# Kernel optimization log

Measured on AMD Instinct MI355X. Metric: run time of the kernel, lower is better.

## Reference

```python
import jax, jax.numpy as jnp
import numpy as np

N_NODES = 50000
N_EDGES = 800000
N_GRAPHS = 512
HID = 128
N_LAYERS = 4
EPS = 1e-4


def setup_inputs() -> dict:
    key = jax.random.key(0)
    ks = jax.random.split(key, 20)
    s = 0.05
    return {
        "z": jax.random.randint(ks[0], (N_NODES,), 0, 100),
        "pos": jax.random.normal(ks[1], (N_NODES, 3), jnp.float32),
        "batch": jnp.sort(jax.random.randint(ks[2], (N_NODES,), 0, N_GRAPHS)),
        "edge_index": jax.random.randint(ks[3], (2, N_EDGES), 0, N_NODES),
        "embed_tab": jax.random.normal(ks[4], (100, HID), jnp.float32) * s,
        "W_pos": jax.random.normal(ks[5], (3, HID), jnp.float32) * s,
        "b_pos": jax.random.normal(ks[6], (HID,), jnp.float32) * s,
        "W_comb": jax.random.normal(ks[7], (2 * HID, HID), jnp.float32) * s,
        "b_comb": jax.random.normal(ks[8], (HID,), jnp.float32) * s,
        "gin_W1": jax.random.normal(ks[9], (N_LAYERS, HID, HID), jnp.float32) * s,
        "gin_b1": jax.random.normal(ks[10], (N_LAYERS, HID), jnp.float32) * s,
        "gin_W2": jax.random.normal(ks[11], (N_LAYERS, HID, HID), jnp.float32) * s,
        "gin_b2": jax.random.normal(ks[12], (N_LAYERS, HID), jnp.float32) * s,
        # heads stacked in order: [alpha, beta, nu, gamma]
        "head_W1": jax.random.normal(ks[13], (4, HID, HID), jnp.float32) * s,
        "head_b1": jax.random.normal(ks[14], (4, HID), jnp.float32) * s,
        "head_W2": jax.random.normal(ks[15], (4, HID, 1), jnp.float32) * s,
        "head_b2": jax.random.normal(ks[16], (4, 1), jnp.float32) * s,
    }


def _forward(z, pos, batch, edge_index, embed_tab, W_pos, b_pos, W_comb, b_comb,
             gin_W1, gin_b1, gin_W2, gin_b2, head_W1, head_b1, head_W2, head_b2):
    # initial embedding: atom embed + linear pos embed -> combine MLP
    atom = embed_tab[z]                                    # [N, H]
    pemb = pos @ W_pos + b_pos                             # [N, H]
    x = jax.nn.relu(jnp.concatenate([atom, pemb], -1) @ W_comb + b_comb)
    src, dst = edge_index[0], edge_index[1]
    # GIN stack: h = MLP(x + sum_{j in N(i)} x_j); ReLU between convs, none after last
    for l in range(N_LAYERS):
        agg = jax.ops.segment_sum(x[src], dst, num_segments=N_NODES)  # [N, H]
        h = x + agg                                        # eps = 0
        h = jax.nn.relu(h @ gin_W1[l] + gin_b1[l]) @ gin_W2[l] + gin_b2[l]
        x = jax.nn.relu(h) if l < N_LAYERS - 1 else h
    # sum pooling per graph
    aggr = jax.ops.segment_sum(x, batch, num_segments=N_GRAPHS)  # [G, F]
    # 4 heads (alpha, beta, nu, gamma), each Linear-ReLU-Linear -> [4, G, 1]
    hh = jax.nn.relu(jnp.einsum('gh,khf->kgf', aggr, head_W1) + head_b1[:, None, :])
    out = jnp.einsum('kgf,kfo->kgo', hh, head_W2) + head_b2[:, None, :]
    alpha = jnp.maximum(jax.nn.softplus(out[0]) + 1.0, 1.0 + EPS)
    beta = jax.nn.softplus(out[1])
    nu = jax.nn.softplus(out[2])
    gamma = out[3]
    aleatoric = beta / (alpha - 1.0)
    epistemic = beta / ((alpha - 1.0) * nu)
    return (gamma, aleatoric, epistemic, nu, alpha, beta)


def reference(z, pos, batch, edge_index, embed_tab, W_pos, b_pos, W_comb, b_comb,
              gin_W1, gin_b1, gin_W2, gin_b2, head_W1, head_b1, head_W2, head_b2):
    return _forward(z, pos, batch, edge_index, embed_tab, W_pos, b_pos, W_comb,
                    b_comb, gin_W1, gin_b1, gin_W2, gin_b2, head_W1, head_b1,
                    head_W2, head_b2)
```

## Files before the change

### kernel.cpp

```cpp
#include <hip/hip_runtime.h>
#include <stdint.h>

#define NN 50000
#define NE 800000
#define NG 512
#define H  128
#define NBK 196
#define EPB 3125

typedef __attribute__((ext_vector_type(8))) short short8;
typedef __attribute__((ext_vector_type(16))) float f32x16;
typedef __attribute__((ext_vector_type(2))) float float2v;

union U4S8 { uint4 u; short8 s; };

__device__ __forceinline__ float softplusf(float x){
    return fmaxf(x, 0.f) + log1pf(expf(-fabsf(x)));
}

__device__ __forceinline__ unsigned rne_bf16_hi(float x){
    unsigned u = __float_as_uint(x);
    unsigned r = u + 0x7fffu + ((u >> 16) & 1u);
    return r & 0xffff0000u;
}

__device__ __forceinline__ void split_pack(float x0, float x1, unsigned &hi, unsigned &lo){
    unsigned h0 = rne_bf16_hi(x0), h1 = rne_bf16_hi(x1);
    hi = (h0 >> 16) | h1;
    float l0 = x0 - __uint_as_float(h0);
    float l1 = x1 - __uint_as_float(h1);
    unsigned g0 = rne_bf16_hi(l0), g1 = rne_bf16_hi(l1);
    lo = (g0 >> 16) | g1;
}

__global__ void k_sentinel(float* out, float val){
    int i = blockIdx.x*256 + threadIdx.x;
    if (i < 6*NG) out[i] = val;
}

__global__ __launch_bounds__(256) void k_pre(
    const float* __restrict__ Wc, uint4* __restrict__ wcf,
    const float* __restrict__ gW1, const float* __restrict__ gW2, uint4* __restrict__ wf,
    const int* __restrict__ ei, int* __restrict__ cnt)
{
    __shared__ int hist[256];
    const int bx = blockIdx.x, t = threadIdx.x;
    if (bx < 16){
        int bid = bx*4 + (t >> 6), lane = t & 63;
        int ntg = bid >> 4, ks = bid & 15;
        int n  = ntg*32 + (lane & 31);
        int kb = ks*16 + (lane >> 5)*8;
        unsigned hi[4], lo[4];
#pragma unroll
        for (int d=0; d<4; d++){
            float x0 = Wc[(size_t)(kb + 2*d    )*H + n];
            float x1 = Wc[(size_t)(kb + 2*d + 1)*H + n];
            split_pack(x0, x1, hi[d], lo[d]);
        }
        wcf[((0*4 + ntg)*16 + ks)*64 + lane] = make_uint4(hi[0],hi[1],hi[2],hi[3]);
        wcf[((1*4 + ntg)*16 + ks)*64 + lane] = make_uint4(lo[0],lo[1],lo[2],lo[3]);
    } else if (bx < 80){
        int bid = (bx-16)*4 + (t >> 6), lane = t & 63;
        int mat = bid >> 5, ntg = (bid >> 3) & 3, ks = bid & 7;
        int l = mat >> 1;
        const float* W = (mat & 1) ? (gW2 + (size_t)l*H*H) : (gW1 + (size_t)l*H*H);
        int n  = ntg*32 + (lane & 31);
        int kb = ks*16 + (lane >> 5)*8;
        unsigned hi[4], lo[4];
#pragma unroll
        for (int d=0; d<4; d++){
            float x0 = W[(size_t)(kb + 2*d    )*H + n];
            float x1 = W[(size_t)(kb + 2*d + 1)*H + n];
            split_pack(x0, x1, hi[d], lo[d]);
        }
        int bh = ((mat*2 + 0)*4 + ntg)*8 + ks;
        int bl = ((mat*2 + 1)*4 + ntg)*8 + ks;
        wf[bh*64 + lane] = make_uint4(hi[0],hi[1],hi[2],hi[3]);
        wf[bl*64 + lane] = make_uint4(lo[0],lo[1],lo[2],lo[3]);
    } else {
        int blk = bx - 80;
        hist[t] = 0;
        __syncthreads();
        int e0 = blk*EPB, e1 = min(e0+EPB, NE);
        for (int e = e0+t; e < e1; e += 256){
            int d = ei[NE+e];
            if ((unsigned)d < NN) atomicAdd(&hist[d>>8], 1);
        }
        __syncthreads();
        if (t < NBK) cnt[t*256 + blk] = hist[t];
    }
}

__global__ __launch_bounds__(256) void k_embed_btot(const int* __restrict__ z,
    const float* __restrict__ pos, const float* __restrict__ emb,
    const float* __restrict__ Wp, const float* __restrict__ bp,
    const float* __restrict__ bc, const uint4* __restrict__ wcf,
    unsigned* __restrict__ xbu,
    const int* __restrict__ cnt, int* __restrict__ tot)
{
    __shared__ unsigned short AhiF[2*8*64*8];
    __shared__ unsigned short AloF[2*8*64*8];
    const int t = threadIdx.x;
    if (blockIdx.x >= 782){
        int* s = (int*)AhiF;
        int k = blockIdx.x - 782;
        s[t] = cnt[k*256 + t];
        __syncthreads();
        for (int sd=128; sd>0; sd>>=1){
            if (t < sd) s[t] += s[t+sd];
            __syncthreads();
        }
        if (t == 0) tot[k] = s[0];
        return;
    }
    const int lane = t & 63, w = t >> 6;
    const int rt = w & 1, cp = w >> 1;
    const int mb = blockIdx.x * 64;
    const int c31 = lane & 31;
    const int q = lane >> 5;

    const int r = t >> 2, c4 = t & 3;
    const int gr = mb + r;
    const int gre = (gr < NN) ? gr : (NN-1);
    const int zr = z[gre];
    const float p0 = pos[gre*3+0], p1 = pos[gre*3+1], p2 = pos[gre*3+2];
    const int rt_s = r >> 5, r31s = r & 31;

    f32x16 acc0, acc1;
#pragma unroll
    for (int i=0;i<16;i++){ acc0[i]=0.f; acc1[i]=0.f; }

#pragma unroll
    for (int kh2=0; kh2<2; kh2++){
        if (kh2) __syncthreads();
#pragma unroll
        for (int i=0;i<8;i++){
            int cl = c4*4 + i*16;
            float4 v;
            if (kh2 == 0){
                v = *(const float4*)(emb + (size_t)zr*H + cl);
            } else {
                float4 w0 = *(const float4*)(Wp + cl);
                float4 w1 = *(const float4*)(Wp + H + cl);
                float4 w2 = *(const float4*)(Wp + 2*H + cl);
                float4 bb = *(const float4*)(bp + cl);
                v.x = p0*w0.x + p1*w1.x + p2*w2.x + bb.x;
                v.y = p0*w0.y + p1*w1.y + p2*w2.y + bb.y;
                v.z = p0*w0.z + p1*w1.z + p2*w2.z + bb.z;
                v.w = p0*w0.w + p1*w1.w + p2*w2.w + bb.w;
            }
            unsigned h0,l0,h1,l1;
            split_pack(v.x, v.y, h0, l0);
            split_pack(v.z, v.w, h1, l1);
            int idx = ((rt_s*8 + (cl>>4))*64 + ((cl>>3)&1)*32 + r31s)*8 + (cl & 7);
            *(uint2*)&AhiF[idx] = make_uint2(h0, h1);
            *(uint2*)&AloF[idx] = make_uint2(l0, l1);
        }
        __syncthreads();
#pragma unroll
        for (int ks=0; ks<8; ks++){
            int ksg = kh2*8 + ks;
            U4S8 ah, al, bh0, bl0, bh1, bl1;
            ah.u  = *(const uint4*)&AhiF[((rt*8+ks)*64 + lane)*8];
            al.u  = *(const uint4*)&AloF[((rt*8+ks)*64 + lane)*8];
            bh0.u = wcf[((0*4 + 2*cp+0)*16 + ksg)*64 + lane];
            bl0.u = wcf[((1*4 + 2*cp+0)*16 + ksg)*64 + lane];
            bh1.u = wcf[((0*4 + 2*cp+1)*16 + ksg)*64 + lane];
            bl1.u = wcf[((1*4 + 2*cp+1)*16 + ksg)*64 + lane];
            acc0 = __builtin_amdgcn_mfma_f32_32x32x16_bf16(ah.s, bh0.s, acc0, 0,0,0);
            acc0 = __builtin_amdgcn_mfma_f32_32x32x16_bf16(ah.s, bl0.s, acc0, 0,0,0);
            acc0 = __builtin_amdgcn_mfma_f32_32x32x16_bf16(al.s, bh0.s, acc0, 0,0,0);
            acc1 = __builtin_amdgcn_mfma_f32_32x32x16_bf16(ah.s, bh1.s, acc1, 0,0,0);
            acc1 = __builtin_amdgcn_mfma_f32_32x32x16_bf16(ah.s, bl1.s, acc1, 0,0,0);
            acc1 = __builtin_amdgcn_mfma_f32_32x32x16_bf16(al.s, bl1.s, acc1, 0,0,0) ,
            acc1 = __builtin_amdgcn_mfma_f32_32x32x16_bf16(al.s, bh1.s, acc1, 0,0,0);
        }
    }

    const float bva = bc[64*cp + c31], bvb = bc[64*cp + 32 + c31];
#pragma unroll
    for (int reg=0; reg<16; reg++){
        int row = 32*rt + (reg & 3) + 8*(reg >> 2) + 4*q;
        int mm = mb + row;
        if (mm < NN){
            float v0 = fmaxf(acc0[reg] + bva, 0.f);
            float v1 = fmaxf(acc1[reg] + bvb, 0.f);
            float pa = __shfl_xor(v0, 1);
            float pb = __shfl_xor(v1, 1);
            unsigned q0 = (unsigned)__builtin_amdgcn_cvt_pk_fp8_f32(v0, pa, 0, false) & 0xffffu;
            unsigned q1 = (unsigned)__builtin_amdgcn_cvt_pk_fp8_f32(v1, pb, 0, false) & 0xffffu;
            unsigned r0 = (unsigned)__shfl_xor((int)q0, 2);
            unsigned r1 = (unsigned)__shfl_xor((int)q1, 2);
            if (!(lane & 3)){
                xbu[(size_t)mm*32 + 16*cp      + (c31>>2)] = q0 | (r0 << 16);
                xbu[(size_t)mm*32 + 16*cp + 8  + (c31>>2)] = q1 | (r1 << 16);
            }
        }
    }
}

__global__ __launch_bounds__(256) void k_soff2(const int* __restrict__ cnt,
    const int* __restrict__ tot, int* __restrict__ soff, int* __restrict__ bb)
{
    __shared__ int P[256], sc[256];
    int k = blockIdx.x, t = threadIdx.x;
    int tv = (t < NBK) ? tot[t] : 0;
    P[t] = tv;
    for (int off=1; off<256; off<<=1){
        __syncthreads();
        int a = (t >= off) ? P[t-off] : 0;
        __syncthreads();
        P[t] += a;
    }
    __syncthreads();
    int bbk = (k == 0) ? 0 : P[k-1];
    if (k == 0){
        if (t == 0) bb[0] = 0;
        if (t < NBK) bb[t+1] = P[t];
    }
    int v = cnt[k*256 + t];
    sc[t] = v;
    for (int off=1; off<256; off<<=1){
        __syncthreads();
        int a = (t >= off) ? sc[t-off] : 0;
        __syncthreads();
        sc[t] += a;
    }
    __syncthreads();
    soff[k*256 + t] = bbk + sc[t] - v;
}

__global__ __launch_bounds__(256) void k_gin_fused(
    const unsigned* __restrict__ xbin,
    const int* __restrict__ iptr, const int* __restrict__ esrc,
    const float* __restrict__ b1, const float* __restrict__ b2,
    const uint4* __restrict__ wf,
    float* __restrict__ xout, unsigned* __restrict__ xbout,
    int l, int relu2, int wx, int wxb)
{
    __shared__ unsigned short AhiF[8*64*8];
    __shared__ unsigned short AloF[8*64*8];
    __shared__ int eS[1024];
    const int t = threadIdx.x, lane = t & 63, w = t >> 6;
    const int mb = blockIdx.x * 32;
    const int c31 = lane & 31;
    const int q = lane >> 5;
    const int c  = lane & 15;
    const int jr = lane >> 4;
    const int ksw = c >> 1, qw = c & 1;

    const uint2* __restrict__ xbp = (const uint2*)xbin;

    const int eTop = (mb + 32 < NN) ? (mb + 32) : NN;
    int e0b = iptr[mb];
    int e1b = iptr[eTop];
    e0b = max(0, min(e0b, NE));
    e1b = max(e0b, min(e1b, NE));
    const int ecnt = e1b - e0b;
    for (int i = t; i < ecnt && i < 1024; i += 256) eS[i] = esrc[e0b + i];
    __syncthreads();
    const int eCap = e0b + 1024;

#define ACC8(U)  { float2v _f; \
    _f = __builtin_amdgcn_cvt_pk_f32_fp8((int)(U).x, false); a0 += _f.x; a1 += _f.y; \
    _f = __builtin_amdgcn_cvt_pk_f32_fp8((int)(U).x, true ); a2 += _f.x; a3 += _f.y; \
    _f = __builtin_amdgcn_cvt_pk_f32_fp8((int)(U).y, false); a4 += _f.x; a5 += _f.y; \
    _f = __builtin_amdgcn_cvt_pk_f32_fp8((int)(U).y, true ); a6 += _f.x; a7 += _f.y; }

#define GLOOP(IX) { \
    for (; j+8 <= e; j += 8){ \
        int i0=IX(j+0), i1=IX(j+1), i2=IX(j+2), i3=IX(j+3); \
        int i4=IX(j+4), i5=IX(j+5), i6=IX(j+6), i7=IX(j+7); \
        uint2 u0 = xbp[(unsigned)i0*16u + c]; \
        uint2 u1 = xbp[(unsigned)i1*16u + c]; \
        uint2 u2 = xbp[(unsigned)i2*16u + c]; \
        uint2 u3 = xbp[(unsigned)i3*16u + c]; \
        uint2 u4 = xbp[(unsigned)i4*16u + c]; \
        uint2 u5 = xbp[(unsigned)i5*16u + c]; \
        uint2 u6 = xbp[(unsigned)i6*16u + c]; \
        uint2 u7 = xbp[(unsigned)i7*16u + c]; \
        ACC8(u0); ACC8(u1); ACC8(u2); ACC8(u3); \
        ACC8(u4); ACC8(u5); ACC8(u6); ACC8(u7); \
    } \
    for (; j+2 <= e; j += 2){ \
        int i0=IX(j+0), i1=IX(j+1); \
        uint2 u0 = xbp[(unsigned)i0*16u + c]; \
        uint2 u1 = xbp[(unsigned)i1*16u + c]; \
        ACC8(u0); ACC8(u1); \
    } \
    if (j < e){ \
        int i0=IX(j); \
        uint2 u0 = xbp[(unsigned)i0*16u + c]; \
        ACC8(u0); \
    } }

#define EIX_L(J) eS[(J) - e0b]
#define EIX_G(J) esrc[(J)]

#pragma unroll
    for (int p=0; p<2; p++){
        int m  = w*8 + p*4 + jr;
        int mm = mb + m;
        int mme = (mm < NN) ? mm : (NN-1);
        int s = iptr[mme], e = iptr[mme+1];
        s = max(0, min(s, NE));
        e = max(s, min(e, NE));
        float a0=0.f,a1=0.f,a2=0.f,a3=0.f,a4=0.f,a5=0.f,a6=0.f,a7=0.f;
        {
            uint2 su = xbp[(size_t)mme*16 + c];
            ACC8(su);
        }
        int j = s;
        if (s >= e0b && e <= eCap){
            GLOOP(EIX_L);
        } else {
            GLOOP(EIX_G);
        }
        unsigned hi4x, hi4y, hi4z, hi4w, lo4x, lo4y, lo4z, lo4w;
        split_pack(a0, a1, hi4x, lo4x);
        split_pack(a2, a3, hi4y, lo4y);
        split_pack(a4, a5, hi4z, lo4z);
        split_pack(a6, a7, hi4w, lo4w);
        int idx = (ksw*64 + qw*32 + (m ^ ksw))*8;
        *(uint4*)&AhiF[idx] = make_uint4(hi4x, hi4y, hi4z, hi4w);
        *(uint4*)&AloF[idx] = make_uint4(lo4x, lo4y, lo4z, lo4w);
    }
#undef EIX_G
#undef EIX_L
#undef GLOOP
#undef ACC8
    __syncthreads();

    const float bv1 = b1[w*32 + c31];
    const float bv2 = b2[w*32 + c31];
    const int mat1 = l*2, mat2 = l*2 + 1;

    f32x16 acc;
#pragma unroll
    for (int i=0;i<16;i++) acc[i] = 0.f;

#pragma unroll
    for (int ks=0; ks<8; ks++){
        U4S8 ah, al, bh, bl;
        ah.u = *(const uint4*)&AhiF[(ks*64 + q*32 + (c31 ^ ks))*8];
        al.u = *(const uint4*)&AloF[(ks*64 + q*32 + (c31 ^ ks))*8];
        bh.u = wf[(((mat1*2+0)*4 + w)*8 + ks)*64 + lane];
        bl.u = wf[(((mat1*2+1)*4 + w)*8 + ks)*64 + lane];
        acc = __builtin_amdgcn_mfma_f32_32x32x16_bf16(ah.s, bh.s, acc, 0,0,0);
        acc = __builtin_amdgcn_mfma_f32_32x32x16_bf16(ah.s, bl.s, acc, 0,0,0);
        acc = __builtin_amdgcn_mfma_f32_32x32x16_bf16(al.s, bh.s, acc, 0,0,0);
    }

    __syncthreads();
    {
        int k   = w*32 + c31;
        int kst = k >> 4, qt = (k >> 3) & 1, jj = k & 7;
#pragma unroll
        for (int reg=0; reg<16; reg++){
            int row = (reg & 3) + 8*(reg >> 2) + 4*q;
            float v = fmaxf(acc[reg] + bv1, 0.f);
            int idx = (kst*64 + qt*32 + (row ^ kst))*8 + jj;
            unsigned hb = rne_bf16_hi(v);
            AhiF[idx] = (unsigned short)(hb >> 16);
            AloF[idx] = (unsigned short)(rne_bf16_hi(v - __uint_as_float(hb)) >> 16);
        }
    }
    __syncthreads();

#pragma unroll
    for (int i=0;i<16;i++) acc[i] = 0.f;
#pragma unroll
    for (int ks=0; ks<8; ks++){
        U4S8 ah, al, bh, bl;
        ah.u = *(const uint4*)&AhiF[(ks*64 + q*32 + (c31 ^ ks))*8];
        al.u = *(const uint4*)&AloF[(ks*64 + q*32 + (c31 ^ ks))*8];
        bh.u = wf[(((mat2*2+0)*4 + w)*8 + ks)*64 + lane];
        bl.u = wf[(((mat2*2+1)*4 + w)*8 + ks)*64 + lane];
        acc = __builtin_amdgcn_mfma_f32_32x32x16_bf16(ah.s, bh.s, acc, 0,0,0);
        acc = __builtin_amdgcn_mfma_f32_32x32x16_bf16(ah.s, bl.s, acc, 0,0,0);
        acc = __builtin_amdgcn_mfma_f32_32x32x16_bf16(al.s, bh.s, acc, 0,0,0);
    }

#pragma unroll
    for (int reg=0; reg<16; reg++){
        int row = (reg & 3) + 8*(reg >> 2) + 4*q;
        int mm = mb + row;
        if (mm < NN){
            float v = acc[reg] + bv2;
            if (relu2) v = fmaxf(v, 0.f);
            if (wx) xout[(size_t)mm*H + w*32 + c31] = v;
            if (wxb){
                float p1 = __shfl_xor(v, 1);
                unsigned qq = (unsigned)__builtin_amdgcn_cvt_pk_fp8_f32(v, p1, 0, false) & 0xffffu;
                unsigned rr = (unsigned)__shfl_xor((int)qq, 2);
                if (!(lane & 3)){
                    xbout[(size_t)mm*32 + w*8 + (c31>>2)] = qq | (rr << 16);
                }
            }
        }
    }
}

__global__ __launch_bounds__(256) void k_part(const int* __restrict__ ei,
    const int* __restrict__ soff, unsigned* __restrict__ tmp)
{
    __shared__ unsigned edgeL[EPB];
    __shared__ int sc[256], startv[256], curv[256];
    __shared__ int tots;
    int blk = blockIdx.x, t = threadIdx.x;
    sc[t] = 0;
    __syncthreads();
    int e0 = blk*EPB, e1 = min(e0+EPB, NE);
    for (int e = e0+t; e < e1; e += 256){
        int d = ei[NE+e];
        if ((unsigned)d < NN) atomicAdd(&sc[d>>8], 1);
    }
    __syncthreads();
    int v = sc[t];
    for (int off=1; off<256; off<<=1){
        __syncthreads();
        int tv = (t >= off) ? sc[t-off] : 0;
        __syncthreads();
        sc[t] += tv;
    }
    __syncthreads();
    startv[t] = sc[t] - v;
    curv[t]   = sc[t] - v;
    if (t == 255) tots = sc[255];
    __syncthreads();
    for (int e = e0+t; e < e1; e += 256){
        int d = ei[NE+e];
        if ((unsigned)d < NN){
            unsigned u = (unsigned)ei[e] | ((unsigned)d << 16);
            int p = atomicAdd(&curv[d>>8], 1);
            edgeL[p] = u;
        }
    }
    __syncthreads();
    int nTot = tots;
    for (int i = t; i < nTot; i += 256){
        unsigned u = edgeL[i];
        int b = u >> 24;
        int g = soff[b*256 + blk] + (i - startv[b]);
        tmp[g] = u;
    }
}

__global__ __launch_bounds__(256) void k_final(const int* __restrict__ bb,
    const unsigned* __restrict__ tmp, int* __restrict__ esrc, int* __restrict__ iptr)
{
    __shared__ int cntN[256], sc[256], curN[256];
    int k = blockIdx.x, t = threadIdx.x;
    int n0 = k*256;
    int nn = min(256, NN - n0);
    int base = bb[k], end = bb[k+1];
    cntN[t] = 0;
    __syncthreads();
    for (int i = base+t; i < end; i += 256){
        int d = (int)(tmp[i] >> 16) - n0;
        if ((unsigned)d < 256u) atomicAdd(&cntN[d], 1);
    }
    __syncthreads();
    int v = cntN[t];
    sc[t] = v;
    for (int off=1; off<256; off<<=1){
        __syncthreads();
        int tv = (t >= off) ? sc[t-off] : 0;
        __syncthreads();
        sc[t] += tv;
    }
    __syncthreads();
    int excl = sc[t] - v;
    curN[t] = excl;
    if (t < nn) iptr[n0 + t] = base + excl;
    if (k == NBK-1 && t == 0) iptr[NN] = end;
    __syncthreads();
    for (int i = base+t; i < end; i += 256){
        unsigned u = tmp[i];
        int d = (int)(u >> 16) - n0;
        if ((unsigned)d < 256u){
            int p = atomicAdd(&curN[d], 1);
            esrc[base + p] = (int)(u & 0xffffu);
        }
    }
}

__global__ __launch_bounds__(256) void k_phe(const float* __restrict__ x,
    const int* __restrict__ batch,
    const float* __restrict__ W1, const float* __restrict__ b1,
    const float* __restrict__ W2, const float* __restrict__ b2,
    float* __restrict__ out)
{
    __shared__ float aggL[128];
    __shared__ float redL[256];
    __shared__ float okL[4];
    int g = blockIdx.x, t = threadIdx.x;
    int c = t & 127, half = t >> 7;
    int lo=0, hi=NN;
    while (lo<hi){ int mid=(lo+hi)>>1; if (batch[mid] < g) lo=mid+1; else hi=mid; }
    int s0 = lo;
    hi = NN;
    while (lo<hi){ int mid=(lo+hi)>>1; if (batch[mid] < g+1) lo=mid+1; else hi=mid; }
    int e0 = lo;
    int n  = e0 - s0;
    int sh = s0 + (half ? (n>>1) : 0);
    int eh = half ? e0 : (s0 + (n>>1));
    float a0=0.f, a1=0.f, a2=0.f, a3=0.f;
    int i = sh;
    for (; i+4 <= eh; i += 4){
        a0 += x[(size_t)(i+0)*H + c];
        a1 += x[(size_t)(i+1)*H + c];
        a2 += x[(size_t)(i+2)*H + c];
        a3 += x[(size_t)(i+3)*H + c];
    }
    for (; i < eh; i++) a0 += x[(size_t)i*H + c];
    float v = (a0+a1) + (a2+a3);
    if (half) redL[c] = v;
    __syncthreads();
    if (!half) aggL[c] = v + redL[c];
    __syncthreads();
    for (int kk = half; kk < 4; kk += 2){
        float acc = b1[kk*H + c];
        const float* wp = W1 + (size_t)kk*H*H + c;
#pragma unroll 8
        for (int qq=0; qq<H; qq++) acc += aggL[qq] * wp[(size_t)qq*H];
        redL[half*128 + c] = fmaxf(acc, 0.f) * W2[kk*H + c];
        __syncthreads();
        for (int sd=64; sd>0; sd>>=1){
            if (c < sd) redL[half*128 + c] += redL[half*128 + c + sd];
            __syncthreads();
        }
        if (c == 0) okL[kk] = redL[half*128];
        __syncthreads();
    }
    if (t == 0){
        float o0 = okL[0] + b2[0];
        float o1 = okL[1] + b2[1];
        float o2 = okL[2] + b2[2];
        float o3 = okL[3] + b2[3];
        float alpha = fmaxf(softplusf(o0) + 1.f, 1.f + 1e-4f);
        float beta  = softplusf(o1);
        float nu    = softplusf(o2);
        float am1   = alpha - 1.f;
        out[0*NG+g] = o3;
        out[1*NG+g] = beta / am1;
        out[2*NG+g] = beta / (am1 * nu);
        out[3*NG+g] = nu;
        out[4*NG+g] = alpha;
        out[5*NG+g] = beta;
    }
}

extern "C" void kernel_launch(void* const* d_in, const int* in_sizes, int n_in,
                              void* d_out, int out_size, void* d_ws, size_t ws_size,
                              hipStream_t stream)
{
    const int*   z     = (const int*)d_in[0];
    const float* pos   = (const float*)d_in[1];
    const int*   batch = (const int*)d_in[2];
    const int*   eidx  = (const int*)d_in[3];
    const float* emb   = (const float*)d_in[4];
    const float* Wp    = (const float*)d_in[5];
    const float* bp    = (const float*)d_in[6];
    const float* Wc    = (const float*)d_in[7];
    const float* bc    = (const float*)d_in[8];
    const float* gW1   = (const float*)d_in[9];
    const float* gb1   = (const float*)d_in[10];
    const float* gW2   = (const float*)d_in[11];
    const float* gb2   = (const float*)d_in[12];
    const float* hW1   = (const float*)d_in[13];
    const float* hb1   = (const float*)d_in[14];
    const float* hW2   = (const float*)d_in[15];
    const float* hb2   = (const float*)d_in[16];
    float* out = (float*)d_out;

    bool ok_sizes = (n_in == 17)
        && in_sizes[0] == NN && in_sizes[1] == NN*3 && in_sizes[2] == NN
        && in_sizes[3] == 2*NE && in_sizes[4] == 100*H
        && in_sizes[7] == 2*H*H && in_sizes[9] == 4*H*H
        && in_sizes[13] == 4*H*H && in_sizes[16] == 4;
    if (!ok_sizes){ k_sentinel<<<12, 256, 0, stream>>>(out, 600000.0f); return; }

    const size_t OFF_XA   = 256;
    const size_t OFF_TMPR = 25600256;
    const size_t OFF_BA   = 51200256;
    const size_t OFF_AGGR = 64000256;
    const size_t OFF_IPTR = 64262400;
    const size_t OFF_ESRC = 64662464;
    const size_t OFF_WF   = 67863296;
    const size_t OFF_WCF  = 68387584;
    const size_t OFF_OK   = 68518656;
    const size_t OFF_BB_B = 68526848;
    const size_t REQ      = 81326848;
    if (ws_size < REQ){ k_sentinel<<<12, 256, 0, stream>>>(out, 500000.0f); return; }

    const size_t OFF_TMP2 = OFF_TMPR;
    const size_t OFF_CNT  = OFF_TMPR + 3200000;
    const size_t OFF_SOFF = OFF_TMPR + 3401216;
    const size_t OFF_TOT  = OFF_TMPR + 3602176;
    const size_t OFF_BBB  = OFF_TMPR + 3603200;

    char* ws = (char*)d_ws;
    float*    xA   = (float*)(ws + OFF_XA);
    unsigned* bA   = (unsigned*)(ws + OFF_BA);
    unsigned* bB   = (unsigned*)(ws + OFF_BB_B);
    int*      iptr = (int*)(ws + OFF_IPTR);
    int*      esrc = (int*)(ws + OFF_ESRC);
    uint4*    wf   = (uint4*)(ws + OFF_WF);
    uint4*    wcf  = (uint4*)(ws + OFF_WCF);
    unsigned* tmp  = (unsigned*)(ws + OFF_TMP2);
    int*      cnt  = (int*)(ws + OFF_CNT);
    int*      soff = (int*)(ws + OFF_SOFF);
    int*      tot  = (int*)(ws + OFF_TOT);
    int*      bb   = (int*)(ws + OFF_BBB);

    k_pre<<<336, 256, 0, stream>>>(Wc, wcf, gW1, gW2, wf, eidx, cnt);
    k_embed_btot<<<978, 256, 0, stream>>>(z, pos, emb, Wp, bp, bc, wcf, bA, cnt, tot);
    k_soff2<<<NBK, 256, 0, stream>>>(cnt, tot, soff, bb);
    k_part <<<256, 256, 0, stream>>>(eidx, soff, tmp);
    k_final<<<NBK, 256, 0, stream>>>(bb, tmp, esrc, iptr);

    unsigned* bi = bA;  unsigned* bo = bB;
    for (int l=0;l<4;l++){
        int wx  = (l == 3) ? 1 : 0;
        int wxb = (l <  3) ? 1 : 0;
        k_gin_fused<<<(NN+31)/32, 256, 0, stream>>>(bi, iptr, esrc,
            gb1 + (size_t)l*H, gb2 + (size_t)l*H, wf, xA, bo, l, (l<3)?1:0, wx, wxb);
        unsigned* bt = bi; bi = bo; bo = bt;
    }

    k_phe<<<NG, 256, 0, stream>>>(xA, batch, hW1, hb1, hW2, hb2, out);
}
```

Measured before the change: 301.8 us.

## Widen GIN gather to 16-byte loads and reuse precomputed bucket counts in partition

The neighbour gather in the fused GIN kernel now has each lane load a 16-byte uint4 (16 fp8 features) instead of 8 bytes. Each lane covers one node row instead of two, and results go to shared memory in a new swizzled layout. The edge-partition kernel now reads per-block bucket counts already computed by the preprocessing kernel instead of recounting destinations with shared-memory atomics. A stray duplicated MFMA (al*bl term) in the embed kernel is also removed, which drops one low-order product. The wider loads cut the number of gather instructions, at the cost of more live accumulator registers per lane.

```diff
diff --git a/kernel.cpp b/kernel.cpp
--- a/kernel.cpp
+++ b/kernel.cpp
@@ -172,7 +172,6 @@
             acc0 = __builtin_amdgcn_mfma_f32_32x32x16_bf16(al.s, bh0.s, acc0, 0,0,0);
             acc1 = __builtin_amdgcn_mfma_f32_32x32x16_bf16(ah.s, bh1.s, acc1, 0,0,0);
             acc1 = __builtin_amdgcn_mfma_f32_32x32x16_bf16(ah.s, bl1.s, acc1, 0,0,0);
-            acc1 = __builtin_amdgcn_mfma_f32_32x32x16_bf16(al.s, bl1.s, acc1, 0,0,0) ,
             acc1 = __builtin_amdgcn_mfma_f32_32x32x16_bf16(al.s, bh1.s, acc1, 0,0,0);
         }
     }
@@ -245,11 +244,11 @@
     const int mb = blockIdx.x * 32;
     const int c31 = lane & 31;
     const int q = lane >> 5;
-    const int c  = lane & 15;
-    const int jr = lane >> 4;
-    const int ksw = c >> 1, qw = c & 1;
-
-    const uint2* __restrict__ xbp = (const uint2*)xbin;
+    const int c8 = lane & 7;
+    const int r8 = lane >> 3;
+    const int m  = w*8 + r8;
+
+    const uint4* __restrict__ xb4 = (const uint4*)xbin;
 
     const int eTop = (mb + 32 < NN) ? (mb + 32) : NN;
     int e0b = iptr[mb];
@@ -261,54 +260,57 @@
     __syncthreads();
     const int eCap = e0b + 1024;
 
-#define ACC8(U)  { float2v _f; \
-    _f = __builtin_amdgcn_cvt_pk_f32_fp8((int)(U).x, false); a0 += _f.x; a1 += _f.y; \
-    _f = __builtin_amdgcn_cvt_pk_f32_fp8((int)(U).x, true ); a2 += _f.x; a3 += _f.y; \
-    _f = __builtin_amdgcn_cvt_pk_f32_fp8((int)(U).y, false); a4 += _f.x; a5 += _f.y; \
-    _f = __builtin_amdgcn_cvt_pk_f32_fp8((int)(U).y, true ); a6 += _f.x; a7 += _f.y; }
+#define ACC16(U) { float2v _f; \
+    _f = __builtin_amdgcn_cvt_pk_f32_fp8((int)(U).x, false); a0  += _f.x; a1  += _f.y; \
+    _f = __builtin_amdgcn_cvt_pk_f32_fp8((int)(U).x, true ); a2  += _f.x; a3  += _f.y; \
+    _f = __builtin_amdgcn_cvt_pk_f32_fp8((int)(U).y, false); a4  += _f.x; a5  += _f.y; \
+    _f = __builtin_amdgcn_cvt_pk_f32_fp8((int)(U).y, true ); a6  += _f.x; a7  += _f.y; \
+    _f = __builtin_amdgcn_cvt_pk_f32_fp8((int)(U).z, false); a8  += _f.x; a9  += _f.y; \
+    _f = __builtin_amdgcn_cvt_pk_f32_fp8((int)(U).z, true ); a10 += _f.x; a11 += _f.y; \
+    _f = __builtin_amdgcn_cvt_pk_f32_fp8((int)(U).w, false); a12 += _f.x; a13 += _f.y; \
+    _f = __builtin_amdgcn_cvt_pk_f32_fp8((int)(U).w, true ); a14 += _f.x; a15 += _f.y; }
 
 #define GLOOP(IX) { \
     for (; j+8 <= e; j += 8){ \
         int i0=IX(j+0), i1=IX(j+1), i2=IX(j+2), i3=IX(j+3); \
         int i4=IX(j+4), i5=IX(j+5), i6=IX(j+6), i7=IX(j+7); \
-        uint2 u0 = xbp[(unsigned)i0*16u + c]; \
-        uint2 u1 = xbp[(unsigned)i1*16u + c]; \
-        uint2 u2 = xbp[(unsigned)i2*16u + c]; \
-        uint2 u3 = xbp[(unsigned)i3*16u + c]; \
-        uint2 u4 = xbp[(unsigned)i4*16u + c]; \
-        uint2 u5 = xbp[(unsigned)i5*16u + c]; \
-        uint2 u6 = xbp[(unsigned)i6*16u + c]; \
-        uint2 u7 = xbp[(unsigned)i7*16u + c]; \
-        ACC8(u0); ACC8(u1); ACC8(u2); ACC8(u3); \
-        ACC8(u4); ACC8(u5); ACC8(u6); ACC8(u7); \
+        uint4 u0 = xb4[(unsigned)i0*8u + c8]; \
+        uint4 u1 = xb4[(unsigned)i1*8u + c8]; \
+        uint4 u2 = xb4[(unsigned)i2*8u + c8]; \
+        uint4 u3 = xb4[(unsigned)i3*8u + c8]; \
+        uint4 u4 = xb4[(unsigned)i4*8u + c8]; \
+        uint4 u5 = xb4[(unsigned)i5*8u + c8]; \
+        uint4 u6 = xb4[(unsigned)i6*8u + c8]; \
+        uint4 u7 = xb4[(unsigned)i7*8u + c8]; \
+        ACC16(u0); ACC16(u1); ACC16(u2); ACC16(u3); \
+        ACC16(u4); ACC16(u5); ACC16(u6); ACC16(u7); \
     } \
     for (; j+2 <= e; j += 2){ \
         int i0=IX(j+0), i1=IX(j+1); \
-        uint2 u0 = xbp[(unsigned)i0*16u + c]; \
-        uint2 u1 = xbp[(unsigned)i1*16u + c]; \
-        ACC8(u0); ACC8(u1); \
+        uint4 u0 = xb4[(unsigned)i0*8u + c8]; \
+        uint4 u1 = xb4[(unsigned)i1*8u + c8]; \
+        ACC16(u0); ACC16(u1); \
     } \
     if (j < e){ \
         int i0=IX(j); \
-        uint2 u0 = xbp[(unsigned)i0*16u + c]; \
-        ACC8(u0); \
+        uint4 u0 = xb4[(unsigned)i0*8u + c8]; \
+        ACC16(u0); \
     } }
 
 #define EIX_L(J) eS[(J) - e0b]
 #define EIX_G(J) esrc[(J)]
 
-#pragma unroll
-    for (int p=0; p<2; p++){
-        int m  = w*8 + p*4 + jr;
-        int mm = mb + m;
-        int mme = (mm < NN) ? mm : (NN-1);
+    {
+        const int mm = mb + m;
+        const int mme = (mm < NN) ? mm : (NN-1);
         int s = iptr[mme], e = iptr[mme+1];
         s = max(0, min(s, NE));
         e = max(s, min(e, NE));
         float a0=0.f,a1=0.f,a2=0.f,a3=0.f,a4=0.f,a5=0.f,a6=0.f,a7=0.f;
+        float a8=0.f,a9=0.f,a10=0.f,a11=0.f,a12=0.f,a13=0.f,a14=0.f,a15=0.f;
         {
-            uint2 su = xbp[(size_t)mme*16 + c];
-            ACC8(su);
+            uint4 su = xb4[(size_t)mme*8 + c8];
+            ACC16(su);
         }
         int j = s;
         if (s >= e0b && e <= eCap){
@@ -316,19 +318,22 @@
         } else {
             GLOOP(EIX_G);
         }
-        unsigned hi4x, hi4y, hi4z, hi4w, lo4x, lo4y, lo4z, lo4w;
-        split_pack(a0, a1, hi4x, lo4x);
-        split_pack(a2, a3, hi4y, lo4y);
-        split_pack(a4, a5, hi4z, lo4z);
-        split_pack(a6, a7, hi4w, lo4w);
-        int idx = (ksw*64 + qw*32 + (m ^ ksw))*8;
-        *(uint4*)&AhiF[idx] = make_uint4(hi4x, hi4y, hi4z, hi4w);
-        *(uint4*)&AloF[idx] = make_uint4(lo4x, lo4y, lo4z, lo4w);
+        unsigned h0,h1,h2,h3,l0,l1,l2,l3;
+        split_pack(a0,a1,h0,l0);  split_pack(a2,a3,h1,l1);
+        split_pack(a4,a5,h2,l2);  split_pack(a6,a7,h3,l3);
+        int idxA = (c8*64 + (m ^ c8))*8;
+        *(uint4*)&AhiF[idxA] = make_uint4(h0,h1,h2,h3);
+        *(uint4*)&AloF[idxA] = make_uint4(l0,l1,l2,l3);
+        split_pack(a8,a9,h0,l0);   split_pack(a10,a11,h1,l1);
+        split_pack(a12,a13,h2,l2); split_pack(a14,a15,h3,l3);
+        int idxB = (c8*64 + 32 + (m ^ c8))*8;
+        *(uint4*)&AhiF[idxB] = make_uint4(h0,h1,h2,h3);
+        *(uint4*)&AloF[idxB] = make_uint4(l0,l1,l2,l3);
     }
 #undef EIX_G
 #undef EIX_L
 #undef GLOOP
-#undef ACC8
+#undef ACC16
     __syncthreads();
 
     const float bv1 = b1[w*32 + c31];
@@ -402,21 +407,14 @@
 }
 
 __global__ __launch_bounds__(256) void k_part(const int* __restrict__ ei,
-    const int* __restrict__ soff, unsigned* __restrict__ tmp)
+    const int* __restrict__ cnt, const int* __restrict__ soff, unsigned* __restrict__ tmp)
 {
     __shared__ unsigned edgeL[EPB];
     __shared__ int sc[256], startv[256], curv[256];
     __shared__ int tots;
     int blk = blockIdx.x, t = threadIdx.x;
-    sc[t] = 0;
-    __syncthreads();
-    int e0 = blk*EPB, e1 = min(e0+EPB, NE);
-    for (int e = e0+t; e < e1; e += 256){
-        int d = ei[NE+e];
-        if ((unsigned)d < NN) atomicAdd(&sc[d>>8], 1);
-    }
-    __syncthreads();
-    int v = sc[t];
+    int v = (t < NBK) ? cnt[t*256 + blk] : 0;
+    sc[t] = v;
     for (int off=1; off<256; off<<=1){
         __syncthreads();
         int tv = (t >= off) ? sc[t-off] : 0;
@@ -428,6 +426,7 @@
     curv[t]   = sc[t] - v;
     if (t == 255) tots = sc[255];
     __syncthreads();
+    int e0 = blk*EPB, e1 = min(e0+EPB, NE);
     for (int e = e0+t; e < e1; e += 256){
         int d = ei[NE+e];
         if ((unsigned)d < NN){
@@ -584,12 +583,10 @@
     const size_t OFF_XA   = 256;
     const size_t OFF_TMPR = 25600256;
     const size_t OFF_BA   = 51200256;
-    const size_t OFF_AGGR = 64000256;
     const size_t OFF_IPTR = 64262400;
     const size_t OFF_ESRC = 64662464;
     const size_t OFF_WF   = 67863296;
     const size_t OFF_WCF  = 68387584;
-    const size_t OFF_OK   = 68518656;
     const size_t OFF_BB_B = 68526848;
     const size_t REQ      = 81326848;
     if (ws_size < REQ){ k_sentinel<<<12, 256, 0, stream>>>(out, 500000.0f); return; }
@@ -617,7 +614,7 @@
     k_pre<<<336, 256, 0, stream>>>(Wc, wcf, gW1, gW2, wf, eidx, cnt);
     k_embed_btot<<<978, 256, 0, stream>>>(z, pos, emb, Wp, bp, bc, wcf, bA, cnt, tot);
     k_soff2<<<NBK, 256, 0, stream>>>(cnt, tot, soff, bb);
-    k_part <<<256, 256, 0, stream>>>(eidx, soff, tmp);
+    k_part <<<256, 256, 0, stream>>>(eidx, cnt, soff, tmp);
     k_final<<<NBK, 256, 0, stream>>>(bb, tmp, esrc, iptr);
 
     unsigned* bi = bA;  unsigned* bo = bB;
```

After: 349.0 us. 15.6% more time.
